# Kernel tuning notes

Measured on AMD Instinct MI355X. Metric: run time of the kernel, lower is better.

## Reference

```python
import jax, jax.numpy as jnp
import numpy as np

NUM_HEADS = 4
D_MODEL = 256
HEAD_DIM = D_MODEL // NUM_HEADS  # 64
B, N = 8, 2048


def _proj(x, W, b):
    # Conv1d with kernel_size=1 == pointwise linear over channel dim
    # x: [B, C_in, N], W: [C_out, C_in], b: [C_out]
    return jnp.einsum('oi,bin->bon', W, x) + b[None, :, None]


def setup_inputs() -> dict:
    key = jax.random.key(0)
    ks = jax.random.split(key, 11)
    s = 1.0 / np.sqrt(D_MODEL)
    return {
        'query': jax.random.normal(ks[0], (B, D_MODEL, N), jnp.float32),
        'key':   jax.random.normal(ks[1], (B, D_MODEL, N), jnp.float32),
        'value': jax.random.normal(ks[2], (B, D_MODEL, N), jnp.float32),
        'Wq': jax.random.normal(ks[3], (D_MODEL, D_MODEL), jnp.float32) * s,
        'bq': jax.random.normal(ks[4], (D_MODEL,), jnp.float32) * 0.01,
        'Wk': jax.random.normal(ks[5], (D_MODEL, D_MODEL), jnp.float32) * s,
        'bk': jax.random.normal(ks[6], (D_MODEL,), jnp.float32) * 0.01,
        'Wv': jax.random.normal(ks[7], (D_MODEL, D_MODEL), jnp.float32) * s,
        'bv': jax.random.normal(ks[8], (D_MODEL,), jnp.float32) * 0.01,
        'Wm': jax.random.normal(ks[9], (D_MODEL, D_MODEL), jnp.float32) * s,
        'bm': jax.random.normal(ks[10], (D_MODEL,), jnp.float32) * 0.01,
    }


def reference(query, key, value, Wq, bq, Wk, bk, Wv, bv, Wm, bm):
    b = query.shape[0]
    # project then split channels into (head_dim, num_heads): [B, d, h, N]
    q = _proj(query, Wq, bq).reshape(b, HEAD_DIM, NUM_HEADS, -1)
    k = _proj(key,   Wk, bk).reshape(b, HEAD_DIM, NUM_HEADS, -1)
    v = _proj(value, Wv, bv).reshape(b, HEAD_DIM, NUM_HEADS, -1)
    scale = 1.0 / jnp.sqrt(jnp.asarray(HEAD_DIM, q.dtype))
    scores = jnp.einsum('bdhn,bdhm->bhnm', q, k) * scale  # [B,H,N,N]
    prob = jax.nn.softmax(scores, axis=-1)
    x = jnp.einsum('bhnm,bdhm->bdhn', prob, v)  # [B,d,H,N]
    x = x.reshape(b, HEAD_DIM * NUM_HEADS, -1)  # [B, d_model, N]
    return _proj(x, Wm, bm)
```

## Files before the change

kernel.cpp:

```cpp
#include <hip/hip_runtime.h>
#include <math.h>


constexpr int BATCH  = 8;
constexpr int DMODEL = 256;
constexpr int SEQ    = 2048;
constexpr int HDIM   = 64;
constexpr int TN     = 128;
constexpr int TM     = 64;
constexpr int NJT    = SEQ / TM;

typedef _Float16 half4_t __attribute__((ext_vector_type(4)));
typedef _Float16 half8_t __attribute__((ext_vector_type(8)));
typedef float    float4_t __attribute__((ext_vector_type(4)));

static __device__ __forceinline__ void ld16_lds(const void* g, void* l) {
    __builtin_amdgcn_global_load_lds(
        (const __attribute__((address_space(1))) unsigned*)g,
        (__attribute__((address_space(3))) unsigned*)l, 16, 0, 0);
}

__global__ __launch_bounds__(256)
void prep_w(const float* __restrict__ Wq, const float* __restrict__ Wk,
            const float* __restrict__ Wv, const float* __restrict__ Wm,
            _Float16* __restrict__ wf)
{
    const int which = blockIdx.y;
    const float* src = which == 0 ? Wq : which == 1 ? Wk : which == 2 ? Wv : Wm;
    const int i = (blockIdx.x * 256 + threadIdx.x) * 4;
    const float4 v = *(const float4*)&src[i];
    half4_t o; o[0] = v.x; o[1] = v.y; o[2] = v.z; o[3] = v.w;
    *(half4_t*)&wf[(size_t)which * DMODEL * DMODEL + i] = o;
}

__global__ __launch_bounds__(256)
void transpose_cvt(const float* __restrict__ q, const float* __restrict__ k,
                   const float* __restrict__ v, _Float16* __restrict__ qx,
                   _Float16* __restrict__ kx, _Float16* __restrict__ vx)
{
    const int n0 = blockIdx.x * 64, c0 = blockIdx.y * 64;
    const int which = blockIdx.z >> 3, b = blockIdx.z & 7;
    const float* X = which == 0 ? q : which == 1 ? k : v;
    _Float16* Y = which == 0 ? qx : which == 1 ? kx : vx;

    __shared__ float T[64][65];
    const int tid = threadIdx.x;
    const int tn = tid & 15, tc = tid >> 4;

    const float* Xb = X + ((size_t)b * DMODEL + c0) * SEQ + n0;
    #pragma unroll
    for (int i = 0; i < 4; ++i) {
        const float4 val = *(const float4*)&Xb[(size_t)(tc + 16 * i) * SEQ + tn * 4];
        T[tc + 16 * i][tn * 4 + 0] = val.x;
        T[tc + 16 * i][tn * 4 + 1] = val.y;
        T[tc + 16 * i][tn * 4 + 2] = val.z;
        T[tc + 16 * i][tn * 4 + 3] = val.w;
    }
    __syncthreads();
    _Float16* Yb = Y + ((size_t)b * SEQ + n0) * DMODEL + c0;
    #pragma unroll
    for (int i = 0; i < 4; ++i) {
        const int n = tc + 16 * i;
        half4_t s4;
        s4[0] = T[tn * 4 + 0][n]; s4[1] = T[tn * 4 + 1][n];
        s4[2] = T[tn * 4 + 2][n]; s4[3] = T[tn * 4 + 3][n];
        *(half4_t*)&Yb[(size_t)n * DMODEL + tn * 4] = s4;
    }
}

__global__ __launch_bounds__(256)
void gemm_qkv(const _Float16* __restrict__ wf, const float* __restrict__ bq,
              const float* __restrict__ bk, const float* __restrict__ bv,
              const _Float16* __restrict__ qx, const _Float16* __restrict__ kx,
              const _Float16* __restrict__ vx, _Float16* __restrict__ qT,
              _Float16* __restrict__ kT, _Float16* __restrict__ vT)
{
    const int n0 = blockIdx.x * 64, m0 = blockIdx.y * 128;
    const int proj = blockIdx.z >> 3, b = blockIdx.z & 7;
    const _Float16* W    = wf + (size_t)proj * DMODEL * DMODEL;
    const float*    bias = proj == 0 ? bq : proj == 1 ? bk : bv;
    const _Float16* X    = proj == 0 ? qx : proj == 1 ? kx : vx;

    const int tid = threadIdx.x, w = tid >> 6, lane = tid & 63;
    const int lm = lane & 15, g = lane >> 4, g8 = g * 8;
    const int cw0 = m0 + w * 32;

    const _Float16* Xb = X + ((size_t)b * SEQ + n0) * DMODEL;

    float4_t acc[2][4];
    #pragma unroll
    for (int mt = 0; mt < 2; ++mt)
        #pragma unroll
        for (int nt = 0; nt < 4; ++nt) acc[mt][nt] = (float4_t){0.f, 0.f, 0.f, 0.f};

    #pragma unroll
    for (int k0 = 0; k0 < DMODEL; k0 += 64) {
        half8_t a[2][2], bb[4][2];
        #pragma unroll
        for (int mt = 0; mt < 2; ++mt)
            #pragma unroll
            for (int kd = 0; kd < 2; ++kd)
                a[mt][kd] = *(const half8_t*)&W[(size_t)(cw0 + mt * 16 + lm) * DMODEL
                                                + k0 + kd * 32 + g8];
        #pragma unroll
        for (int nt = 0; nt < 4; ++nt)
            #pragma unroll
            for (int kd = 0; kd < 2; ++kd)
                bb[nt][kd] = *(const half8_t*)&Xb[(size_t)(nt * 16 + lm) * DMODEL
                                                  + k0 + kd * 32 + g8];
        #pragma unroll
        for (int kd = 0; kd < 2; ++kd)
            #pragma unroll
            for (int mt = 0; mt < 2; ++mt)
                #pragma unroll
                for (int nt = 0; nt < 4; ++nt)
                    acc[mt][nt] = __builtin_amdgcn_mfma_f32_16x16x32_f16(
                        a[mt][kd], bb[nt][kd], acc[mt][nt], 0, 0, 0);
    }

    __shared__ _Float16 Tw[4][64][36];
    #pragma unroll
    for (int mt = 0; mt < 2; ++mt) {
        const float4 b4 = *(const float4*)&bias[cw0 + mt * 16 + g * 4];
        const float bb4[4] = {b4.x, b4.y, b4.z, b4.w};
        #pragma unroll
        for (int nt = 0; nt < 4; ++nt) {
            half4_t pk;
            #pragma unroll
            for (int r = 0; r < 4; ++r) pk[r] = (_Float16)(acc[mt][nt][r] + bb4[r]);
            *(half4_t*)&Tw[w][nt * 16 + lm][mt * 16 + g * 4] = pk;
        }
    }

    if (proj < 2) {
        _Float16* dst = (proj == 0 ? qT : kT);
        const int dbase = cw0 >> 2;
        const int cchunk = dbase >> 3;
        const int h2 = lane >> 4, lml = lane & 15;
        #pragma unroll
        for (int it = 0; it < 4; ++it) {
            const int nl = it * 16 + lml;
            half8_t chunk;
            #pragma unroll
            for (int dl = 0; dl < 8; ++dl) chunk[dl] = Tw[w][nl][4 * dl + h2];
            const size_t off = ((size_t)(b * 4 + h2) * SEQ + n0 + nl) * HDIM
                               + ((cchunk ^ (nl & 7)) << 3);
            *(half8_t*)&dst[off] = chunk;
        }
    } else {
        const int u = lane >> 1, half_ = lane & 1;
        const int hh = u & 3, dl = u >> 2;
        const int d = (cw0 >> 2) + dl;
        const size_t rowbase =
            (((size_t)(b * 4 + hh) * NJT + (n0 >> 6)) * HDIM + d) * (size_t)TM;
        #pragma unroll
        for (int it = 0; it < 4; ++it) {
            const int jc = half_ * 4 + it;
            half8_t ch;
            #pragma unroll
            for (int e = 0; e < 8; ++e) ch[e] = Tw[w][jc * 8 + e][4 * dl + hh];
            *(half8_t*)&vT[rowbase + ((jc ^ dl) << 3)] = ch;
        }
    }
}

__global__ __launch_bounds__(256, 2)
void attn_f16(const _Float16* __restrict__ qT, const _Float16* __restrict__ kT,
              const _Float16* __restrict__ vT, _Float16* __restrict__ xT)
{
    const int bh = blockIdx.y, b = bh >> 2, h = bh & 3;
    const int tid = threadIdx.x, wid = tid >> 6, lane = tid & 63;
    const int lm = lane & 15, g = lane >> 4;
    const int i0 = blockIdx.x * TN + wid * 32;

    __shared__ _Float16 Kb[2][TM * HDIM];
    __shared__ _Float16 Vb[2][TM * HDIM];

    half8_t bq[2][2];
    const _Float16* qbase = qT + (size_t)bh * SEQ * HDIM;
    #pragma unroll
    for (int rt = 0; rt < 2; ++rt)
        #pragma unroll
        for (int kd = 0; kd < 2; ++kd) {
            const int row = i0 + rt * 16 + lm;
            half8_t r8 = *(const half8_t*)(qbase + (size_t)row * HDIM
                                           + (((kd * 4 + g) ^ (lm & 7)) << 3));
            #pragma unroll
            for (int e = 0; e < 8; ++e) r8[e] = r8[e] * (_Float16)0.125f;
            bq[rt][kd] = r8;
        }

    const char* kt = (const char*)(kT + (size_t)bh * SEQ * HDIM);
    const char* vt = (const char*)(vT + (size_t)bh * NJT * TM * HDIM);

    float4_t o[2][4];
    #pragma unroll
    for (int rt = 0; rt < 2; ++rt)
        #pragma unroll
        for (int dt = 0; dt < 4; ++dt) o[rt][dt] = (float4_t){0.f, 0.f, 0.f, 0.f};
    float rs[2] = {0.f, 0.f};

    #define STAGE(jt, bu)                                                     \
        {                                                                     \
            const char* kg = kt + (size_t)(jt) * 8192;                        \
            const char* vg = vt + (size_t)(jt) * 8192;                        \
            _Pragma("unroll")                                                 \
            for (int p = 0; p < 2; ++p) {                                     \
                const int c = wid + p * 4;                                    \
                ld16_lds(kg + c * 1024 + lane * 16, (char*)&Kb[bu][0] + c * 1024); \
                ld16_lds(vg + c * 1024 + lane * 16, (char*)&Vb[bu][0] + c * 1024); \
            }                                                                 \
        }

    STAGE(0, 0);
    __syncthreads();

    for (int jt = 0; jt < NJT; ++jt) {
        const int cur = jt & 1;
        if (jt + 1 < NJT) STAGE(jt + 1, cur ^ 1);

        float4_t s[4][2];
        #pragma unroll
        for (int ct = 0; ct < 4; ++ct)
            #pragma unroll
            for (int rt = 0; rt < 2; ++rt) s[ct][rt] = (float4_t){0.f, 0.f, 0.f, 0.f};
        #pragma unroll
        for (int kd = 0; kd < 2; ++kd)
            #pragma unroll
            for (int ct = 0; ct < 4; ++ct) {
                const half8_t fk = *(const half8_t*)
                    &Kb[cur][(ct * 16 + lm) * HDIM + (((kd * 4 + g) ^ (lm & 7)) << 3)];
                #pragma unroll
                for (int rt = 0; rt < 2; ++rt)
                    s[ct][rt] = __builtin_amdgcn_mfma_f32_16x16x32_f16(
                        fk, bq[rt][kd], s[ct][rt], 0, 0, 0);
            }

        half4_t ap[4][2];
        #pragma unroll
        for (int ct = 0; ct < 4; ++ct)
            #pragma unroll
            for (int rt = 0; rt < 2; ++rt)
                #pragma unroll
                for (int r = 0; r < 4; ++r) {
                    const float p = __expf(s[ct][rt][r]);
                    rs[rt] += p;
                    ap[ct][rt][r] = (_Float16)p;
                }

        #pragma unroll
        for (int ct = 0; ct < 4; ++ct)
            #pragma unroll
            for (int dt = 0; dt < 4; ++dt) {
                const int d = dt * 16 + lm;
                const half4_t fv = *(const half4_t*)
                    &Vb[cur][d * TM + ((((ct * 2 + (g >> 1)) ^ (lm & 7)) << 3)
                                       + ((g & 1) << 2))];
                #pragma unroll
                for (int rt = 0; rt < 2; ++rt)
                    o[rt][dt] = __builtin_amdgcn_mfma_f32_16x16x16f16(
                        ap[ct][rt], fv, o[rt][dt], 0, 0, 0);
            }
        __syncthreads();
    }

    #pragma unroll
    for (int rt = 0; rt < 2; ++rt) {
        rs[rt] += __shfl_xor(rs[rt], 16);
        rs[rt] += __shfl_xor(rs[rt], 32);
    }
    #pragma unroll
    for (int rt = 0; rt < 2; ++rt) {
        float inv[4];
        #pragma unroll
        for (int r = 0; r < 4; ++r) inv[r] = 1.0f / __shfl(rs[rt], 4 * g + r);
        #pragma unroll
        for (int dt = 0; dt < 4; ++dt) {
            const int c = 4 * (dt * 16 + lm) + h;
            #pragma unroll
            for (int r = 0; r < 4; ++r) {
                const int n = i0 + rt * 16 + 4 * g + r;
                xT[((size_t)b * SEQ + n) * DMODEL + c] = (_Float16)(o[rt][dt][r] * inv[r]);
            }
        }
    }
    #undef STAGE
}

__global__ __launch_bounds__(256)
void gemm_final(const _Float16* __restrict__ wm, const float* __restrict__ bias,
                const _Float16* __restrict__ xT, float* __restrict__ out)
{
    const int n0 = blockIdx.x * 64, m0 = blockIdx.y * 128;
    const int b = blockIdx.z;
    const int tid = threadIdx.x, w = tid >> 6, lane = tid & 63;
    const int lm = lane & 15, g = lane >> 4, g8 = g * 8;
    const int cw0 = m0 + w * 32;

    const _Float16* Xb = xT + ((size_t)b * SEQ + n0) * DMODEL;

    float4_t acc[2][4];
    #pragma unroll
    for (int mt = 0; mt < 2; ++mt)
        #pragma unroll
        for (int nt = 0; nt < 4; ++nt) acc[mt][nt] = (float4_t){0.f, 0.f, 0.f, 0.f};

    #pragma unroll
    for (int k0 = 0; k0 < DMODEL; k0 += 64) {
        half8_t a[2][2], bb[4][2];
        #pragma unroll
        for (int mt = 0; mt < 2; ++mt)
            #pragma unroll
            for (int kd = 0; kd < 2; ++kd)
                a[mt][kd] = *(const half8_t*)&wm[(size_t)(cw0 + mt * 16 + lm) * DMODEL
                                                 + k0 + kd * 32 + g8];
        #pragma unroll
        for (int nt = 0; nt < 4; ++nt)
            #pragma unroll
            for (int kd = 0; kd < 2; ++kd)
                bb[nt][kd] = *(const half8_t*)&Xb[(size_t)(nt * 16 + lm) * DMODEL
                                                  + k0 + kd * 32 + g8];
        #pragma unroll
        for (int kd = 0; kd < 2; ++kd)
            #pragma unroll
            for (int mt = 0; mt < 2; ++mt)
                #pragma unroll
                for (int nt = 0; nt < 4; ++nt)
                    acc[mt][nt] = __builtin_amdgcn_mfma_f32_16x16x32_f16(
                        a[mt][kd], bb[nt][kd], acc[mt][nt], 0, 0, 0);
    }

    #pragma unroll
    for (int mt = 0; mt < 2; ++mt)
        #pragma unroll
        for (int r = 0; r < 4; ++r) {
            const int co = cw0 + mt * 16 + g * 4 + r;
            const float bv_ = bias[co];
            #pragma unroll
            for (int nt = 0; nt < 4; ++nt)
                out[((size_t)b * DMODEL + co) * SEQ + n0 + nt * 16 + lm] =
                    acc[mt][nt][r] + bv_;
        }
}

extern "C" void kernel_launch(void* const* d_in, const int* in_sizes, int n_in,
                              void* d_out, int out_size, void* d_ws, size_t ws_size,
                              hipStream_t stream) {
    const float* query = (const float*)d_in[0];
    const float* key_  = (const float*)d_in[1];
    const float* value = (const float*)d_in[2];
    const float* Wq = (const float*)d_in[3];  const float* bq = (const float*)d_in[4];
    const float* Wk = (const float*)d_in[5];  const float* bk = (const float*)d_in[6];
    const float* Wv = (const float*)d_in[7];  const float* bv = (const float*)d_in[8];
    const float* Wm = (const float*)d_in[9];  const float* bm = (const float*)d_in[10];
    float* out = (float*)d_out;

    const size_t bufElems = (size_t)BATCH * DMODEL * SEQ;
    _Float16* qx = (_Float16*)d_ws;
    _Float16* kx = qx + bufElems;
    _Float16* vx = kx + bufElems;
    _Float16* qT = vx + bufElems;
    _Float16* kT = qT + bufElems;
    _Float16* vT = kT + bufElems;
    _Float16* wf = vT + bufElems;
    _Float16* xT = qx;

    prep_w<<<dim3(DMODEL * DMODEL / 1024, 4), 256, 0, stream>>>(Wq, Wk, Wv, Wm, wf);
    transpose_cvt<<<dim3(SEQ / 64, DMODEL / 64, 3 * BATCH), 256, 0, stream>>>(
        query, key_, value, qx, kx, vx);
    gemm_qkv<<<dim3(SEQ / 64, 2, 3 * BATCH), 256, 0, stream>>>(
        wf, bq, bk, bv, qx, kx, vx, qT, kT, vT);
    attn_f16<<<dim3(SEQ / TN, BATCH * 4), 256, 0, stream>>>(qT, kT, vT, xT);
    gemm_final<<<dim3(SEQ / 64, 2, BATCH), 256, 0, stream>>>(
        wf + (size_t)3 * DMODEL * DMODEL, bm, xT, out);
}
```

Before: 217.3 us.

## Fuse input transpose into QKV GEMM and split attention over key halves

Removes the separate transpose/convert kernel by having the QKV projection load fp32 inputs, transpose and convert them through LDS, and compute all 256 output channels per block. Attention is split into two key-range halves per query tile for more parallelism, with row sums computed via an MFMA against a ones vector. Partial outputs and sums go to workspace, and the final GEMM merges and normalizes them. This adds extra writes and reads of a second partial buffer. With no running max it relies on unnormalized exp sums, which already held before.

```diff
diff --git a/kernel.cpp b/kernel.cpp
--- a/kernel.cpp
+++ b/kernel.cpp
@@ -33,71 +33,64 @@
     *(half4_t*)&wf[(size_t)which * DMODEL * DMODEL + i] = o;
 }
 
-__global__ __launch_bounds__(256)
-void transpose_cvt(const float* __restrict__ q, const float* __restrict__ k,
-                   const float* __restrict__ v, _Float16* __restrict__ qx,
-                   _Float16* __restrict__ kx, _Float16* __restrict__ vx)
-{
-    const int n0 = blockIdx.x * 64, c0 = blockIdx.y * 64;
-    const int which = blockIdx.z >> 3, b = blockIdx.z & 7;
-    const float* X = which == 0 ? q : which == 1 ? k : v;
-    _Float16* Y = which == 0 ? qx : which == 1 ? kx : vx;
-
-    __shared__ float T[64][65];
-    const int tid = threadIdx.x;
-    const int tn = tid & 15, tc = tid >> 4;
-
-    const float* Xb = X + ((size_t)b * DMODEL + c0) * SEQ + n0;
-    #pragma unroll
-    for (int i = 0; i < 4; ++i) {
-        const float4 val = *(const float4*)&Xb[(size_t)(tc + 16 * i) * SEQ + tn * 4];
-        T[tc + 16 * i][tn * 4 + 0] = val.x;
-        T[tc + 16 * i][tn * 4 + 1] = val.y;
-        T[tc + 16 * i][tn * 4 + 2] = val.z;
-        T[tc + 16 * i][tn * 4 + 3] = val.w;
-    }
-    __syncthreads();
-    _Float16* Yb = Y + ((size_t)b * SEQ + n0) * DMODEL + c0;
-    #pragma unroll
-    for (int i = 0; i < 4; ++i) {
-        const int n = tc + 16 * i;
-        half4_t s4;
-        s4[0] = T[tn * 4 + 0][n]; s4[1] = T[tn * 4 + 1][n];
-        s4[2] = T[tn * 4 + 2][n]; s4[3] = T[tn * 4 + 3][n];
-        *(half4_t*)&Yb[(size_t)n * DMODEL + tn * 4] = s4;
-    }
-}
-
-__global__ __launch_bounds__(256)
+__global__ __launch_bounds__(256, 3)
 void gemm_qkv(const _Float16* __restrict__ wf, const float* __restrict__ bq,
               const float* __restrict__ bk, const float* __restrict__ bv,
-              const _Float16* __restrict__ qx, const _Float16* __restrict__ kx,
-              const _Float16* __restrict__ vx, _Float16* __restrict__ qT,
+              const float* __restrict__ Xq, const float* __restrict__ Xk,
+              const float* __restrict__ Xv, _Float16* __restrict__ qT,
               _Float16* __restrict__ kT, _Float16* __restrict__ vT)
 {
-    const int n0 = blockIdx.x * 64, m0 = blockIdx.y * 128;
-    const int proj = blockIdx.z >> 3, b = blockIdx.z & 7;
+    const int n0 = blockIdx.x * 64;
+    const int proj = blockIdx.y >> 3, b = blockIdx.y & 7;
     const _Float16* W    = wf + (size_t)proj * DMODEL * DMODEL;
     const float*    bias = proj == 0 ? bq : proj == 1 ? bk : bv;
-    const _Float16* X    = proj == 0 ? qx : proj == 1 ? kx : vx;
-
-    const int tid = threadIdx.x, w = tid >> 6, lane = tid & 63;
+    const float*    X    = (proj == 0 ? Xq : proj == 1 ? Xk : Xv)
+                           + (size_t)b * DMODEL * SEQ;
+
+    __shared__ __align__(16) char lds[50432];
+    float*    T  = (float*)lds;
+    _Float16* Xs = (_Float16*)(lds + 16640);
+    _Float16* Tw = (_Float16*)lds;
+
+    const int tid = threadIdx.x, tn = tid & 15, tc = tid >> 4;
+
+    #pragma unroll
+    for (int cc = 0; cc < 4; ++cc) {
+        __syncthreads();
+        #pragma unroll
+        for (int i = 0; i < 4; ++i) {
+            const int c = tc + 16 * i;
+            const float4 v = *(const float4*)&X[(size_t)(cc * 64 + c) * SEQ + n0 + tn * 4];
+            T[c * 65 + tn * 4 + 0] = v.x; T[c * 65 + tn * 4 + 1] = v.y;
+            T[c * 65 + tn * 4 + 2] = v.z; T[c * 65 + tn * 4 + 3] = v.w;
+        }
+        __syncthreads();
+        #pragma unroll
+        for (int i = 0; i < 4; ++i) {
+            const int n = tc + 16 * i;
+            half4_t h4;
+            #pragma unroll
+            for (int j = 0; j < 4; ++j) h4[j] = (_Float16)T[(tn * 4 + j) * 65 + n];
+            *(half4_t*)&Xs[n * 264 + cc * 64 + tn * 4] = h4;
+        }
+    }
+    __syncthreads();
+
+    const int w = tid >> 6, lane = tid & 63;
     const int lm = lane & 15, g = lane >> 4, g8 = g * 8;
-    const int cw0 = m0 + w * 32;
-
-    const _Float16* Xb = X + ((size_t)b * SEQ + n0) * DMODEL;
-
-    float4_t acc[2][4];
-    #pragma unroll
-    for (int mt = 0; mt < 2; ++mt)
+    const int cw0 = w * 64;
+
+    float4_t acc[4][4];
+    #pragma unroll
+    for (int mt = 0; mt < 4; ++mt)
         #pragma unroll
         for (int nt = 0; nt < 4; ++nt) acc[mt][nt] = (float4_t){0.f, 0.f, 0.f, 0.f};
 
     #pragma unroll
     for (int k0 = 0; k0 < DMODEL; k0 += 64) {
-        half8_t a[2][2], bb[4][2];
-        #pragma unroll
-        for (int mt = 0; mt < 2; ++mt)
+        half8_t a[4][2], bb[4][2];
+        #pragma unroll
+        for (int mt = 0; mt < 4; ++mt)
             #pragma unroll
             for (int kd = 0; kd < 2; ++kd)
                 a[mt][kd] = *(const half8_t*)&W[(size_t)(cw0 + mt * 16 + lm) * DMODEL
@@ -106,21 +99,21 @@
         for (int nt = 0; nt < 4; ++nt)
             #pragma unroll
             for (int kd = 0; kd < 2; ++kd)
-                bb[nt][kd] = *(const half8_t*)&Xb[(size_t)(nt * 16 + lm) * DMODEL
+                bb[nt][kd] = *(const half8_t*)&Xs[(nt * 16 + lm) * 264
                                                   + k0 + kd * 32 + g8];
         #pragma unroll
         for (int kd = 0; kd < 2; ++kd)
             #pragma unroll
-            for (int mt = 0; mt < 2; ++mt)
+            for (int mt = 0; mt < 4; ++mt)
                 #pragma unroll
                 for (int nt = 0; nt < 4; ++nt)
                     acc[mt][nt] = __builtin_amdgcn_mfma_f32_16x16x32_f16(
                         a[mt][kd], bb[nt][kd], acc[mt][nt], 0, 0, 0);
     }
-
-    __shared__ _Float16 Tw[4][64][36];
-    #pragma unroll
-    for (int mt = 0; mt < 2; ++mt) {
+    __syncthreads();
+
+    #pragma unroll
+    for (int mt = 0; mt < 4; ++mt) {
         const float4 b4 = *(const float4*)&bias[cw0 + mt * 16 + g * 4];
         const float bb4[4] = {b4.x, b4.y, b4.z, b4.w};
         #pragma unroll
@@ -128,47 +121,50 @@
             half4_t pk;
             #pragma unroll
             for (int r = 0; r < 4; ++r) pk[r] = (_Float16)(acc[mt][nt][r] + bb4[r]);
-            *(half4_t*)&Tw[w][nt * 16 + lm][mt * 16 + g * 4] = pk;
+            *(half4_t*)&Tw[((w * 64 + nt * 16 + lm)) * 68 + mt * 16 + g * 4] = pk;
         }
     }
 
     if (proj < 2) {
         _Float16* dst = (proj == 0 ? qT : kT);
-        const int dbase = cw0 >> 2;
-        const int cchunk = dbase >> 3;
         const int h2 = lane >> 4, lml = lane & 15;
         #pragma unroll
         for (int it = 0; it < 4; ++it) {
             const int nl = it * 16 + lml;
-            half8_t chunk;
-            #pragma unroll
-            for (int dl = 0; dl < 8; ++dl) chunk[dl] = Tw[w][nl][4 * dl + h2];
-            const size_t off = ((size_t)(b * 4 + h2) * SEQ + n0 + nl) * HDIM
-                               + ((cchunk ^ (nl & 7)) << 3);
-            *(half8_t*)&dst[off] = chunk;
+            #pragma unroll
+            for (int dc = 0; dc < 2; ++dc) {
+                half8_t ch;
+                #pragma unroll
+                for (int e = 0; e < 8; ++e)
+                    ch[e] = Tw[(w * 64 + nl) * 68 + 4 * (dc * 8 + e) + h2];
+                const int chunk = (w * 2 + dc) ^ (nl & 7);
+                *(half8_t*)&dst[((size_t)(b * 4 + h2) * SEQ + n0 + nl) * HDIM
+                                + chunk * 8] = ch;
+            }
         }
     } else {
-        const int u = lane >> 1, half_ = lane & 1;
-        const int hh = u & 3, dl = u >> 2;
-        const int d = (cw0 >> 2) + dl;
+        const int hh = lane & 3, dl = (lane >> 2) & 15;
+        const int d = w * 16 + dl;
         const size_t rowbase =
             (((size_t)(b * 4 + hh) * NJT + (n0 >> 6)) * HDIM + d) * (size_t)TM;
         #pragma unroll
-        for (int it = 0; it < 4; ++it) {
-            const int jc = half_ * 4 + it;
+        for (int jc = 0; jc < 8; ++jc) {
             half8_t ch;
             #pragma unroll
-            for (int e = 0; e < 8; ++e) ch[e] = Tw[w][jc * 8 + e][4 * dl + hh];
-            *(half8_t*)&vT[rowbase + ((jc ^ dl) << 3)] = ch;
-        }
-    }
-}
-
-__global__ __launch_bounds__(256, 2)
+            for (int e = 0; e < 8; ++e)
+                ch[e] = Tw[(w * 64 + jc * 8 + e) * 68 + 4 * dl + hh];
+            *(half8_t*)&vT[rowbase + ((jc ^ (dl & 7)) << 3)] = ch;
+        }
+    }
+}
+
+__global__ __launch_bounds__(256, 4)
 void attn_f16(const _Float16* __restrict__ qT, const _Float16* __restrict__ kT,
-              const _Float16* __restrict__ vT, _Float16* __restrict__ xT)
+              const _Float16* __restrict__ vT, _Float16* __restrict__ xa,
+              _Float16* __restrict__ xb, float* __restrict__ rs)
 {
-    const int bh = blockIdx.y, b = bh >> 2, h = bh & 3;
+    const int bh = blockIdx.z, b = bh >> 2, h = bh & 3;
+    const int jh = blockIdx.y;
     const int tid = threadIdx.x, wid = tid >> 6, lane = tid & 63;
     const int lm = lane & 15, g = lane >> 4;
     const int i0 = blockIdx.x * TN + wid * 32;
@@ -190,15 +186,17 @@
             bq[rt][kd] = r8;
         }
 
-    const char* kt = (const char*)(kT + (size_t)bh * SEQ * HDIM);
-    const char* vt = (const char*)(vT + (size_t)bh * NJT * TM * HDIM);
-
-    float4_t o[2][4];
-    #pragma unroll
-    for (int rt = 0; rt < 2; ++rt)
+    const char* kt = (const char*)(kT + ((size_t)bh * SEQ + jh * (SEQ / 2)) * HDIM);
+    const char* vt = (const char*)(vT + ((size_t)bh * NJT + jh * 16) * TM * HDIM);
+
+    float4_t o[2][4], o5[2];
+    #pragma unroll
+    for (int rt = 0; rt < 2; ++rt) {
         #pragma unroll
         for (int dt = 0; dt < 4; ++dt) o[rt][dt] = (float4_t){0.f, 0.f, 0.f, 0.f};
-    float rs[2] = {0.f, 0.f};
+        o5[rt] = (float4_t){0.f, 0.f, 0.f, 0.f};
+    }
+    const half4_t vone = {(_Float16)1.f, (_Float16)1.f, (_Float16)1.f, (_Float16)1.f};
 
     #define STAGE(jt, bu)                                                     \
         {                                                                     \
@@ -215,9 +213,9 @@
     STAGE(0, 0);
     __syncthreads();
 
-    for (int jt = 0; jt < NJT; ++jt) {
+    for (int jt = 0; jt < 16; ++jt) {
         const int cur = jt & 1;
-        if (jt + 1 < NJT) STAGE(jt + 1, cur ^ 1);
+        if (jt + 1 < 16) STAGE(jt + 1, cur ^ 1);
 
         float4_t s[4][2];
         #pragma unroll
@@ -242,11 +240,14 @@
             #pragma unroll
             for (int rt = 0; rt < 2; ++rt)
                 #pragma unroll
-                for (int r = 0; r < 4; ++r) {
-                    const float p = __expf(s[ct][rt][r]);
-                    rs[rt] += p;
-                    ap[ct][rt][r] = (_Float16)p;
-                }
+                for (int r = 0; r < 4; ++r)
+                    ap[ct][rt][r] = (_Float16)__expf(s[ct][rt][r]);
+        #pragma unroll
+        for (int ct = 0; ct < 4; ++ct)
+            #pragma unroll
+            for (int rt = 0; rt < 2; ++rt)
+                o5[rt] = __builtin_amdgcn_mfma_f32_16x16x16f16(
+                    ap[ct][rt], vone, o5[rt], 0, 0, 0);
 
         #pragma unroll
         for (int ct = 0; ct < 4; ++ct)
@@ -264,32 +265,33 @@
         __syncthreads();
     }
 
-    #pragma unroll
-    for (int rt = 0; rt < 2; ++rt) {
-        rs[rt] += __shfl_xor(rs[rt], 16);
-        rs[rt] += __shfl_xor(rs[rt], 32);
-    }
-    #pragma unroll
-    for (int rt = 0; rt < 2; ++rt) {
-        float inv[4];
-        #pragma unroll
-        for (int r = 0; r < 4; ++r) inv[r] = 1.0f / __shfl(rs[rt], 4 * g + r);
+    _Float16* xp = jh ? xb : xa;
+    #pragma unroll
+    for (int rt = 0; rt < 2; ++rt)
         #pragma unroll
         for (int dt = 0; dt < 4; ++dt) {
             const int c = 4 * (dt * 16 + lm) + h;
             #pragma unroll
             for (int r = 0; r < 4; ++r) {
                 const int n = i0 + rt * 16 + 4 * g + r;
-                xT[((size_t)b * SEQ + n) * DMODEL + c] = (_Float16)(o[rt][dt][r] * inv[r]);
-            }
-        }
+                xp[((size_t)b * SEQ + n) * DMODEL + c] = (_Float16)o[rt][dt][r];
+            }
+        }
+    if (lm == 0) {
+        #pragma unroll
+        for (int rt = 0; rt < 2; ++rt)
+            #pragma unroll
+            for (int r = 0; r < 4; ++r)
+                rs[((size_t)jh * 32 + bh) * SEQ + i0 + rt * 16 + 4 * g + r] =
+                    o5[rt][r];
     }
     #undef STAGE
 }
 
 __global__ __launch_bounds__(256)
 void gemm_final(const _Float16* __restrict__ wm, const float* __restrict__ bias,
-                const _Float16* __restrict__ xT, float* __restrict__ out)
+                const _Float16* __restrict__ xa, const _Float16* __restrict__ xb,
+                const float* __restrict__ rs, float* __restrict__ out)
 {
     const int n0 = blockIdx.x * 64, m0 = blockIdx.y * 128;
     const int b = blockIdx.z;
@@ -297,7 +299,21 @@
     const int lm = lane & 15, g = lane >> 4, g8 = g * 8;
     const int cw0 = m0 + w * 32;
 
-    const _Float16* Xb = xT + ((size_t)b * SEQ + n0) * DMODEL;
+    const _Float16* Xa = xa + ((size_t)b * SEQ + n0) * DMODEL;
+    const _Float16* Xb2 = xb + ((size_t)b * SEQ + n0) * DMODEL;
+
+    half8_t pm[4];
+    #pragma unroll
+    for (int nt = 0; nt < 4; ++nt) {
+        const int n = n0 + nt * 16 + lm;
+        #pragma unroll
+        for (int hh = 0; hh < 4; ++hh) {
+            const float l = rs[(size_t)(b * 4 + hh) * SEQ + n]
+                          + rs[(size_t)(32 + b * 4 + hh) * SEQ + n];
+            const _Float16 iv = (_Float16)(1.0f / l);
+            pm[nt][hh] = iv; pm[nt][hh + 4] = iv;
+        }
+    }
 
     float4_t acc[2][4];
     #pragma unroll
@@ -317,9 +333,12 @@
         #pragma unroll
         for (int nt = 0; nt < 4; ++nt)
             #pragma unroll
-            for (int kd = 0; kd < 2; ++kd)
-                bb[nt][kd] = *(const half8_t*)&Xb[(size_t)(nt * 16 + lm) * DMODEL
-                                                  + k0 + kd * 32 + g8];
+            for (int kd = 0; kd < 2; ++kd) {
+                const size_t off = (size_t)(nt * 16 + lm) * DMODEL + k0 + kd * 32 + g8;
+                const half8_t va = *(const half8_t*)&Xa[off];
+                const half8_t vb = *(const half8_t*)&Xb2[off];
+                bb[nt][kd] = (va + vb) * pm[nt];
+            }
         #pragma unroll
         for (int kd = 0; kd < 2; ++kd)
             #pragma unroll
@@ -356,21 +375,18 @@
     float* out = (float*)d_out;
 
     const size_t bufElems = (size_t)BATCH * DMODEL * SEQ;
-    _Float16* qx = (_Float16*)d_ws;
-    _Float16* kx = qx + bufElems;
-    _Float16* vx = kx + bufElems;
-    _Float16* qT = vx + bufElems;
+    _Float16* qT = (_Float16*)d_ws;
     _Float16* kT = qT + bufElems;
     _Float16* vT = kT + bufElems;
-    _Float16* wf = vT + bufElems;
-    _Float16* xT = qx;
+    _Float16* xa = vT + bufElems;
+    _Float16* xb = xa + bufElems;
+    _Float16* wf = xb + bufElems;
+    float*    rsb = (float*)(wf + 4 * DMODEL * DMODEL);
 
     prep_w<<<dim3(DMODEL * DMODEL / 1024, 4), 256, 0, stream>>>(Wq, Wk, Wv, Wm, wf);
-    transpose_cvt<<<dim3(SEQ / 64, DMODEL / 64, 3 * BATCH), 256, 0, stream>>>(
-        query, key_, value, qx, kx, vx);
-    gemm_qkv<<<dim3(SEQ / 64, 2, 3 * BATCH), 256, 0, stream>>>(
-        wf, bq, bk, bv, qx, kx, vx, qT, kT, vT);
-    attn_f16<<<dim3(SEQ / TN, BATCH * 4), 256, 0, stream>>>(qT, kT, vT, xT);
+    gemm_qkv<<<dim3(SEQ / 64, 3 * BATCH), 256, 0, stream>>>(
+        wf, bq, bk, bv, query, key_, value, qT, kT, vT);
+    attn_f16<<<dim3(SEQ / TN, 2, BATCH * 4), 256, 0, stream>>>(qT, kT, vT, xa, xb, rsb);
     gemm_final<<<dim3(SEQ / 64, 2, BATCH), 256, 0, stream>>>(
-        wf + (size_t)3 * DMODEL * DMODEL, bm, xT, out);
-}
+        wf + (size_t)3 * DMODEL * DMODEL, bm, xa, xb, rsb, out);
+}
```

Result: faster. 195.4 us (-10.1%).
